# Kernel tuning notes

Measured on AMD Instinct MI355X. Metric: run time of the kernel, lower is better.

## Reference

```python
import jax, jax.numpy as jnp
import numpy as np

N_NODES = 50000
N_EDGES = 800000
IN_FEATS = 128
N_HIDDEN = 128
N_CLASSES = 64


def setup_inputs() -> dict:
    key = jax.random.key(0)
    ks = jax.random.split(key, 12)
    x = jax.random.normal(ks[0], (N_NODES, IN_FEATS), dtype=jnp.float32)
    src = jax.random.randint(ks[1], (N_EDGES,), 0, N_NODES, dtype=jnp.int32)
    dst = jax.random.randint(ks[2], (N_EDGES,), 0, N_NODES, dtype=jnp.int32)
    dims = [(IN_FEATS, N_HIDDEN), (N_HIDDEN, N_HIDDEN), (N_HIDDEN, N_CLASSES)]
    inp = {"x": x, "src": src, "dst": dst}
    for i, (din, dout) in enumerate(dims):
        s = (2.0 / (din + dout)) ** 0.5  # xavier-ish init scale
        inp[f"Wself{i}"] = jax.random.normal(ks[3 + 3 * i], (din, dout), dtype=jnp.float32) * s
        inp[f"Wneigh{i}"] = jax.random.normal(ks[4 + 3 * i], (din, dout), dtype=jnp.float32) * s
        inp[f"b{i}"] = jnp.zeros((dout,), dtype=jnp.float32)
    return inp


def _sage_conv(h, src, dst, inv_deg, Wself, Wneigh, b):
    # mean aggregation over in-neighbors: gather on src, segment-sum on dst
    agg = jax.ops.segment_sum(h[src], dst, num_segments=N_NODES)  # [N, d]
    h_neigh = agg * inv_deg[:, None]
    return h @ Wself + h_neigh @ Wneigh + b


def reference(x, src, dst, Wself0, Wneigh0, b0, Wself1, Wneigh1, b1, Wself2, Wneigh2, b2):
    # in-degree (clamped to 1, matching DGL mean aggregator), shared across layers
    deg = jax.ops.segment_sum(jnp.ones((N_EDGES,), dtype=jnp.float32), dst, num_segments=N_NODES)
    inv_deg = 1.0 / jnp.maximum(deg, 1.0)
    # dropout is identity in eval mode
    h = _sage_conv(x, src, dst, inv_deg, Wself0, Wneigh0, b0)
    h = jax.nn.relu(h)
    h = _sage_conv(h, src, dst, inv_deg, Wself1, Wneigh1, b1)
    h = jax.nn.relu(h)
    h = _sage_conv(h, src, dst, inv_deg, Wself2, Wneigh2, b2)
    return h
```

## Files before the change

### kernel.cpp

```cpp
#include <hip/hip_runtime.h>

#define N_NODES 50000
#define N_EDGES 800000
#define NB_SCAN 196
#define NODES_PER_GRP 6250
#define BUCKET_CAP 131072
#define CAST_BLOCKS 6250

typedef unsigned short ushort_t;
typedef __attribute__((ext_vector_type(8))) short  short8v;
typedef __attribute__((ext_vector_type(4))) float  float4v;
typedef __attribute__((ext_vector_type(4))) unsigned short ushort4v;
typedef __attribute__((ext_vector_type(8))) unsigned short ushort8v;
typedef __attribute__((ext_vector_type(4))) int int4v;

__device__ __forceinline__ ushort_t f2bf(float f) {
    unsigned u = __float_as_uint(f);
    unsigned r = 0x7fffu + ((u >> 16) & 1u);
    return (ushort_t)((u + r) >> 16);
}
__device__ __forceinline__ float bf2f(ushort_t h) {
    return __uint_as_float((unsigned)h << 16);
}

__global__ __launch_bounds__(256) void cast_pack_k(const float* __restrict__ x,
                                                   ushort_t* __restrict__ xb,
                                                   int* __restrict__ bcur,
                                                   const float* __restrict__ W0n, const float* __restrict__ W0s,
                                                   const float* __restrict__ W1n, const float* __restrict__ W1s,
                                                   const float* __restrict__ W2n, const float* __restrict__ W2s,
                                                   ushort_t* __restrict__ P) {
    const int b = blockIdx.x, t = threadIdx.x;
    if (b < CAST_BLOCKS) {
        int i = b * 256 + t;
        if (i < N_NODES * 32) {
            float4 v = ((const float4*)x)[i];
            ushort4v h;
            h[0] = f2bf(v.x); h[1] = f2bf(v.y); h[2] = f2bf(v.z); h[3] = f2bf(v.w);
            ((ushort4v*)xb)[i] = h;
        }
        if (i < 8) bcur[i] = 0;
        return;
    }
    int tid = (b - CAST_BLOCKS) * 256 + t;
    const float* W; int dout; int base; int r;
    if      (tid < 2048)  { W = W0n; dout = 128; base = 0;     r = tid; }
    else if (tid < 4096)  { W = W0s; dout = 128; base = 16384; r = tid - 2048; }
    else if (tid < 6144)  { W = W1n; dout = 128; base = 32768; r = tid - 4096; }
    else if (tid < 8192)  { W = W1s; dout = 128; base = 49152; r = tid - 6144; }
    else if (tid < 9216)  { W = W2n; dout = 64;  base = 65536; r = tid - 8192; }
    else                  { W = W2s; dout = 64;  base = 73728; r = tid - 9216; }
    int lane = r & 63;
    int ks = (r >> 6) & 3;
    int nt = r >> 8;
    int col = nt * 16 + (lane & 15);
    int k0 = ks * 32 + ((lane >> 4) << 3);
    ushort_t* d = P + (size_t)base + (size_t)r * 8;
    ushort4v lo4, hi4;
#pragma unroll
    for (int j = 0; j < 4; ++j) lo4[j] = f2bf(W[(size_t)(k0 + j) * dout + col]);
#pragma unroll
    for (int j = 0; j < 4; ++j) hi4[j] = f2bf(W[(size_t)(k0 + 4 + j) * dout + col]);
    *(ushort4v*)d = lo4;
    *(ushort4v*)(d + 4) = hi4;
}

__global__ __launch_bounds__(256) void bucket_k(const int4v* __restrict__ dst4,
                                                const int4v* __restrict__ src4,
                                                int* __restrict__ bcur,
                                                int2* __restrict__ buckets) {
    __shared__ int lcount[8];
    __shared__ int lbase[8];
    const int t = threadIdx.x, b = blockIdx.x;
    if (t < 8) lcount[t] = 0;
    __syncthreads();

    const int idx = b * 256 + t;
    int4v d, s;
    if (idx < N_EDGES / 4) {
        d = __builtin_nontemporal_load(dst4 + idx);
        s = __builtin_nontemporal_load(src4 + idx);
    } else {
        d[0] = d[1] = d[2] = d[3] = -1;
        s[0] = s[1] = s[2] = s[3] = 0;
    }
    int g[4], li[4];
#pragma unroll
    for (int j = 0; j < 4; ++j) {
        int dv = d[j];
        g[j] = (dv >= 0) ? (dv / NODES_PER_GRP) : -1;
        li[j] = (g[j] >= 0) ? atomicAdd(&lcount[g[j]], 1) : 0;
    }
    __syncthreads();
    if (t < 8) lbase[t] = atomicAdd(bcur + t, lcount[t]);
    __syncthreads();
#pragma unroll
    for (int j = 0; j < 4; ++j) {
        if (g[j] >= 0) {
            int pos = lbase[g[j]] + li[j];
            buckets[(size_t)g[j] * BUCKET_CAP + pos] = make_int2(d[j], s[j]);
        }
    }
}

__global__ __launch_bounds__(1024) void deg_hist_k(const int* __restrict__ bcur,
                                                   const int2* __restrict__ buckets,
                                                   int* __restrict__ deg) {
    __shared__ int hist[NODES_PER_GRP];
    const int g = blockIdx.x;
    const int t = threadIdx.x;
    const int lo = g * NODES_PER_GRP;
    const int cnt = bcur[g];
    const int2* bk = buckets + (size_t)g * BUCKET_CAP;
    for (int i = t; i < NODES_PER_GRP; i += 1024) hist[i] = 0;
    __syncthreads();
    for (int i = t; i < cnt; i += 1024) {
        atomicAdd(&hist[bk[i].x - lo], 1);
    }
    __syncthreads();
    for (int i = t; i < NODES_PER_GRP; i += 1024) deg[lo + i] = hist[i];
}

__global__ __launch_bounds__(256) void block_sum_k(const int* __restrict__ deg,
                                                   int* __restrict__ bsum, int n) {
    __shared__ int s[256];
    int t = threadIdx.x, b = blockIdx.x;
    int i = b * 256 + t;
    s[t] = (i < n) ? deg[i] : 0;
    __syncthreads();
#pragma unroll
    for (int off = 128; off > 0; off >>= 1) {
        if (t < off) s[t] += s[t + off];
        __syncthreads();
    }
    if (t == 0) bsum[b] = s[0];
}

__global__ __launch_bounds__(256) void rowptr_fused_k(const int* __restrict__ deg,
                                                      const int* __restrict__ bsum,
                                                      int* __restrict__ rowptr,
                                                      int* __restrict__ cursor,
                                                      float* __restrict__ inv) {
    __shared__ int sb[256];
    __shared__ int s[256];
    const int t = threadIdx.x, b = blockIdx.x;
    int v = (t < NB_SCAN) ? bsum[t] : 0;
    sb[t] = v;
    __syncthreads();
#pragma unroll
    for (int off = 1; off < 256; off <<= 1) {
        int u = (t >= off) ? sb[t - off] : 0;
        __syncthreads();
        sb[t] += u;
        __syncthreads();
    }
    const int boffb = (b == 0) ? 0 : sb[b - 1];
    if (b == NB_SCAN - 1 && t == 0) rowptr[N_NODES] = sb[NB_SCAN - 1];

    int i = b * 256 + t;
    int d = (i < N_NODES) ? deg[i] : 0;
    s[t] = d;
    __syncthreads();
#pragma unroll
    for (int off = 1; off < 256; off <<= 1) {
        int u = (t >= off) ? s[t - off] : 0;
        __syncthreads();
        s[t] += u;
        __syncthreads();
    }
    if (i < N_NODES) {
        int r = boffb + s[t] - d;
        rowptr[i] = r;
        cursor[i] = r;
        inv[i] = 1.0f / fmaxf((float)d, 1.0f);
    }
}

__global__ __launch_bounds__(256) void scatter_bucket_k(const int* __restrict__ bcur,
                                                        const int2* __restrict__ buckets,
                                                        int* __restrict__ cursor,
                                                        int* __restrict__ csr) {
    const int grp = blockIdx.x & 7;
    const int cnt = bcur[grp];
    const int2* bk = buckets + (size_t)grp * BUCKET_CAP;
    const int stride = (gridDim.x >> 3) * 256;
    for (int i = (blockIdx.x >> 3) * 256 + threadIdx.x; i < cnt; i += stride) {
        int2 e = bk[i];
        csr[atomicAdd(cursor + e.x, 1)] = e.y;
    }
}

__global__ __launch_bounds__(256) void aggm_k(const ushort_t* __restrict__ h,
                                              const int* __restrict__ rowptr,
                                              const int* __restrict__ csr,
                                              const float* __restrict__ inv,
                                              ushort_t* __restrict__ m, int N) {
    int node = (blockIdx.x * 256 + threadIdx.x) >> 4;
    int c = threadIdx.x & 15;
    if (node >= N) return;
    int start = rowptr[node], end = rowptr[node + 1];

    const ushort8v* hp = (const ushort8v*)h;
    float a0[8] = {}, a1[8] = {}, a2[8] = {}, a3[8] = {};
    int j = start;
    for (; j + 3 < end; j += 4) {
        int u0 = csr[j], u1 = csr[j + 1], u2 = csr[j + 2], u3 = csr[j + 3];
        ushort8v w0 = hp[(size_t)u0 * 16 + c];
        ushort8v w1 = hp[(size_t)u1 * 16 + c];
        ushort8v w2 = hp[(size_t)u2 * 16 + c];
        ushort8v w3 = hp[(size_t)u3 * 16 + c];
#pragma unroll
        for (int k = 0; k < 8; ++k) {
            a0[k] += bf2f(w0[k]); a1[k] += bf2f(w1[k]);
            a2[k] += bf2f(w2[k]); a3[k] += bf2f(w3[k]);
        }
    }
    for (; j < end; ++j) {
        ushort8v w = hp[(size_t)csr[j] * 16 + c];
#pragma unroll
        for (int k = 0; k < 8; ++k) a0[k] += bf2f(w[k]);
    }
    float s = inv[node];
    ushort8v o;
#pragma unroll
    for (int k = 0; k < 8; ++k) o[k] = f2bf(((a0[k] + a1[k]) + (a2[k] + a3[k])) * s);
    __builtin_nontemporal_store(o, (ushort8v*)m + (size_t)node * 16 + c);
}

__global__ __launch_bounds__(256, 4) void fusedgemm_k(const ushort_t* __restrict__ H,
                                                      const ushort_t* __restrict__ M,
                                                      const short8v* __restrict__ Ws,
                                                      const short8v* __restrict__ Wn,
                                                      const float* __restrict__ bias,
                                                      ushort_t* __restrict__ Out, int N) {
    __shared__ ushort_t sm[2][64 * 128];
    char* sbH = (char*)sm[0];
    char* sbM = (char*)sm[1];
    const int bm = blockIdx.x * 64;
    const int t = threadIdx.x;
    const int w = t >> 6, l = t & 63;

    {
        const ushort8v* Hp = (const ushort8v*)H;
        const ushort8v* Mp = (const ushort8v*)M;
        ushort8v zeroV = {0, 0, 0, 0, 0, 0, 0, 0};
#pragma unroll
        for (int it = 0; it < 4; ++it) {
            int r = it * 16 + (t >> 4);
            int row = bm + r;
            int byte = (r * 256 + (t & 15) * 16) ^ ((r & 7) << 4);
            ushort8v vh = zeroV, vm = zeroV;
            if (row < N) {
                vh = Hp[(size_t)row * 16 + (t & 15)];
                vm = __builtin_nontemporal_load(Mp + (size_t)row * 16 + (t & 15));
            }
            *(ushort8v*)(sbH + byte) = vh;
            *(ushort8v*)(sbM + byte) = vm;
        }
    }
    __syncthreads();

    float bv[8];
#pragma unroll
    for (int nt = 0; nt < 8; ++nt) bv[nt] = bias[nt * 16 + (l & 15)];

    float4v acc[8] = {};
#pragma unroll
    for (int ks = 0; ks < 4; ++ks) {
        int r0 = w * 16 + (l & 15);
        int b0 = (r0 * 256 + ks * 64 + (l >> 4) * 16) ^ ((r0 & 7) << 4);
        short8v ah = *(const short8v*)(sbH + b0);
        short8v am = *(const short8v*)(sbM + b0);
#pragma unroll
        for (int nt = 0; nt < 8; ++nt) {
            short8v bs = Ws[(nt * 4 + ks) * 64 + l];
            short8v bn = Wn[(nt * 4 + ks) * 64 + l];
            acc[nt] = __builtin_amdgcn_mfma_f32_16x16x32_bf16(ah, bs, acc[nt], 0, 0, 0);
            acc[nt] = __builtin_amdgcn_mfma_f32_16x16x32_bf16(am, bn, acc[nt], 0, 0, 0);
        }
    }

#pragma unroll
    for (int i = 0; i < 4; ++i) {
        int row = bm + w * 16 + (l >> 4) * 4 + i;
        if (row < N) {
#pragma unroll
            for (int nt = 0; nt < 8; ++nt) {
                int col = nt * 16 + (l & 15);
                Out[(size_t)row * 128 + col] = f2bf(fmaxf(acc[nt][i] + bv[nt], 0.f));
            }
        }
    }
}

__global__ __launch_bounds__(256, 4) void dual64_k(const ushort_t* __restrict__ A,
                                                   const short8v* __restrict__ Wn,
                                                   const short8v* __restrict__ Ws,
                                                   const float* __restrict__ bias,
                                                   ushort_t* __restrict__ Z,
                                                   float* __restrict__ S, int N) {
    constexpr int NT = 4;
    __shared__ ushort_t Asm[64 * 128];
    char* sb = (char*)Asm;
    const int bm = blockIdx.x * 64;
    const int t = threadIdx.x;
    const int w = t >> 6, l = t & 63;

    {
        const ushort8v* Ap = (const ushort8v*)A;
        ushort8v zeroV = {0, 0, 0, 0, 0, 0, 0, 0};
#pragma unroll
        for (int it = 0; it < 4; ++it) {
            int r = it * 16 + (t >> 4);
            int row = bm + r;
            ushort8v v = zeroV;
            if (row < N) v = Ap[(size_t)row * 16 + (t & 15)];
            int byte = (r * 256 + (t & 15) * 16) ^ ((r & 7) << 4);
            *(ushort8v*)(sb + byte) = v;
        }
    }
    __syncthreads();

    float bv[NT];
#pragma unroll
    for (int nt = 0; nt < NT; ++nt) bv[nt] = bias[nt * 16 + (l & 15)];

    float4v accS[NT] = {}, accN[NT] = {};
#pragma unroll
    for (int ks = 0; ks < 4; ++ks) {
        int r0 = w * 16 + (l & 15);
        int b0 = (r0 * 256 + ks * 64 + (l >> 4) * 16) ^ ((r0 & 7) << 4);
        short8v a = *(const short8v*)(sb + b0);
#pragma unroll
        for (int nt = 0; nt < NT; ++nt) {
            short8v bs = Ws[(nt * 4 + ks) * 64 + l];
            short8v bn = Wn[(nt * 4 + ks) * 64 + l];
            accS[nt] = __builtin_amdgcn_mfma_f32_16x16x32_bf16(a, bs, accS[nt], 0, 0, 0);
            accN[nt] = __builtin_amdgcn_mfma_f32_16x16x32_bf16(a, bn, accN[nt], 0, 0, 0);
        }
    }

#pragma unroll
    for (int i = 0; i < 4; ++i) {
        int row = bm + w * 16 + (l >> 4) * 4 + i;
        if (row < N) {
#pragma unroll
            for (int nt = 0; nt < NT; ++nt) {
                int col = nt * 16 + (l & 15);
                S[(size_t)row * 64 + col] = accS[nt][i] + bv[nt];
                Z[(size_t)row * 64 + col] = f2bf(accN[nt][i]);
            }
        }
    }
}

__global__ __launch_bounds__(256) void agg64_k(const ushort_t* __restrict__ z,
                                               const int* __restrict__ rowptr,
                                               const int* __restrict__ csr,
                                               const float* __restrict__ inv,
                                               float* __restrict__ out, int N) {
    int node = (blockIdx.x * 256 + threadIdx.x) >> 3;
    int c = threadIdx.x & 7;
    if (node >= N) return;
    int start = rowptr[node], end = rowptr[node + 1];

    const ushort8v* zp = (const ushort8v*)z;
    float a0[8] = {}, a1[8] = {}, a2[8] = {}, a3[8] = {};
    int j = start;
    for (; j + 3 < end; j += 4) {
        int u0 = csr[j], u1 = csr[j + 1], u2 = csr[j + 2], u3 = csr[j + 3];
        ushort8v w0 = zp[(size_t)u0 * 8 + c];
        ushort8v w1 = zp[(size_t)u1 * 8 + c];
        ushort8v w2 = zp[(size_t)u2 * 8 + c];
        ushort8v w3 = zp[(size_t)u3 * 8 + c];
#pragma unroll
        for (int k = 0; k < 8; ++k) {
            a0[k] += bf2f(w0[k]); a1[k] += bf2f(w1[k]);
            a2[k] += bf2f(w2[k]); a3[k] += bf2f(w3[k]);
        }
    }
    for (; j < end; ++j) {
        ushort8v w = zp[(size_t)csr[j] * 8 + c];
#pragma unroll
        for (int k = 0; k < 8; ++k) a0[k] += bf2f(w[k]);
    }
    float s = inv[node];
    float* op = out + (size_t)node * 64 + c * 8;
    float4 o0 = *(float4*)op;
    float4 o1 = *(float4*)(op + 4);
    o0.x += ((a0[0] + a1[0]) + (a2[0] + a3[0])) * s;
    o0.y += ((a0[1] + a1[1]) + (a2[1] + a3[1])) * s;
    o0.z += ((a0[2] + a1[2]) + (a2[2] + a3[2])) * s;
    o0.w += ((a0[3] + a1[3]) + (a2[3] + a3[3])) * s;
    o1.x += ((a0[4] + a1[4]) + (a2[4] + a3[4])) * s;
    o1.y += ((a0[5] + a1[5]) + (a2[5] + a3[5])) * s;
    o1.z += ((a0[6] + a1[6]) + (a2[6] + a3[6])) * s;
    o1.w += ((a0[7] + a1[7]) + (a2[7] + a3[7])) * s;
    *(float4*)op = o0;
    *(float4*)(op + 4) = o1;
}


extern "C" void kernel_launch(void* const* d_in, const int* in_sizes, int n_in,
                              void* d_out, int out_size, void* d_ws, size_t ws_size,
                              hipStream_t stream) {
    const float* x       = (const float*)d_in[0];
    const int*   src     = (const int*)d_in[1];
    const int*   dst     = (const int*)d_in[2];
    const float* Wself0  = (const float*)d_in[3];
    const float* Wneigh0 = (const float*)d_in[4];
    const float* b0      = (const float*)d_in[5];
    const float* Wself1  = (const float*)d_in[6];
    const float* Wneigh1 = (const float*)d_in[7];
    const float* b1      = (const float*)d_in[8];
    const float* Wself2  = (const float*)d_in[9];
    const float* Wneigh2 = (const float*)d_in[10];
    const float* b2      = (const float*)d_in[11];
    float* out = (float*)d_out;

    char* ws = (char*)d_ws;
    size_t off = 0;
    auto alloc = [&](size_t bytes) -> void* {
        void* p = ws + off;
        off += (bytes + 255) & ~(size_t)255;
        return p;
    };
    int*      deg     = (int*)alloc((size_t)N_NODES * 4);
    float*    inv     = (float*)alloc((size_t)N_NODES * 4);
    int*      rowptr  = (int*)alloc((size_t)(N_NODES + 1) * 4);
    int*      cursor  = (int*)alloc((size_t)N_NODES * 4);
    int*      csr     = (int*)alloc((size_t)N_EDGES * 4);
    int*      bsum    = (int*)alloc((size_t)NB_SCAN * 4);
    int*      bcur    = (int*)alloc((size_t)8 * 4);
    int2*     buckets = (int2*)alloc((size_t)8 * BUCKET_CAP * 8);
    ushort_t* packW   = (ushort_t*)alloc((size_t)81920 * 2);
    ushort_t* xb      = (ushort_t*)alloc((size_t)N_NODES * 128 * 2);
    ushort_t* mbuf    = (ushort_t*)alloc((size_t)N_NODES * 128 * 2);
    ushort_t* h1      = (ushort_t*)alloc((size_t)N_NODES * 128 * 2);
    ushort_t* h2      = (ushort_t*)alloc((size_t)N_NODES * 128 * 2);
    ushort_t* z64     = (ushort_t*)alloc((size_t)N_NODES * 64 * 2);

    dim3 b256(256);
    const int gemmBlocks   = (N_NODES + 63) / 64;
    const int aggmBlocks   = (N_NODES * 16 + 255) / 256;
    const int agg64Blocks  = (N_NODES * 8 + 255) / 256;
    const int bucketBlocks = (N_EDGES / 4 + 255) / 256;

    cast_pack_k<<<CAST_BLOCKS + 40, b256, 0, stream>>>(x, xb, bcur,
                                                       Wneigh0, Wself0, Wneigh1, Wself1,
                                                       Wneigh2, Wself2, packW);
    bucket_k<<<bucketBlocks, b256, 0, stream>>>((const int4v*)dst, (const int4v*)src,
                                                bcur, buckets);
    deg_hist_k<<<8, dim3(1024), 0, stream>>>(bcur, buckets, deg);
    block_sum_k<<<NB_SCAN, b256, 0, stream>>>(deg, bsum, N_NODES);
    rowptr_fused_k<<<NB_SCAN, b256, 0, stream>>>(deg, bsum, rowptr, cursor, inv);
    scatter_bucket_k<<<512, b256, 0, stream>>>(bcur, buckets, cursor, csr);

    const short8v* pN0 = (const short8v*)(packW);
    const short8v* pS0 = (const short8v*)(packW + 16384);
    const short8v* pN1 = (const short8v*)(packW + 32768);
    const short8v* pS1 = (const short8v*)(packW + 49152);
    const short8v* pN2 = (const short8v*)(packW + 65536);
    const short8v* pS2 = (const short8v*)(packW + 73728);

    aggm_k<<<aggmBlocks, b256, 0, stream>>>(xb, rowptr, csr, inv, mbuf, N_NODES);
    fusedgemm_k<<<gemmBlocks, b256, 0, stream>>>(xb, mbuf, pS0, pN0, b0, h1, N_NODES);

    aggm_k<<<aggmBlocks, b256, 0, stream>>>(h1, rowptr, csr, inv, mbuf, N_NODES);
    fusedgemm_k<<<gemmBlocks, b256, 0, stream>>>(h1, mbuf, pS1, pN1, b1, h2, N_NODES);

    dual64_k<<<gemmBlocks, b256, 0, stream>>>(h2, pN2, pS2, b2, z64, out, N_NODES);
    agg64_k<<<agg64Blocks, b256, 0, stream>>>(z64, rowptr, csr, inv, out, N_NODES);
}
```

Measured before the change: 218.3 us.

## Fuse neighbor mean-aggregation into GEMM kernel and fold block sums into histogram

Replaces the separate aggregation kernel plus GEMM with one kernel that gathers and averages neighbor rows directly into shared memory before the MFMA loop, eliminating the intermediate aggregated buffer write and read and one launch per layer. Also computes the per-256-node degree block sums inside the histogram kernel by regrouping nodes into 6400-node buckets, removing the block_sum kernel. The fused kernel runs the irregular gather with fewer blocks and serializes gather with compute, which may reduce latency hiding.

```diff
diff --git a/kernel.cpp b/kernel.cpp
--- a/kernel.cpp
+++ b/kernel.cpp
@@ -3,7 +3,8 @@
 #define N_NODES 50000
 #define N_EDGES 800000
 #define NB_SCAN 196
-#define NODES_PER_GRP 6250
+#define NODES_PER_GRP 6400
+#define CHUNKS_PER_GRP 25
 #define BUCKET_CAP 131072
 #define CAST_BLOCKS 6250
 
@@ -105,7 +106,8 @@
 
 __global__ __launch_bounds__(1024) void deg_hist_k(const int* __restrict__ bcur,
                                                    const int2* __restrict__ buckets,
-                                                   int* __restrict__ deg) {
+                                                   int* __restrict__ deg,
+                                                   int* __restrict__ bsum) {
     __shared__ int hist[NODES_PER_GRP];
     const int g = blockIdx.x;
     const int t = threadIdx.x;
@@ -118,22 +120,17 @@
         atomicAdd(&hist[bk[i].x - lo], 1);
     }
     __syncthreads();
-    for (int i = t; i < NODES_PER_GRP; i += 1024) deg[lo + i] = hist[i];
-}
-
-__global__ __launch_bounds__(256) void block_sum_k(const int* __restrict__ deg,
-                                                   int* __restrict__ bsum, int n) {
-    __shared__ int s[256];
-    int t = threadIdx.x, b = blockIdx.x;
-    int i = b * 256 + t;
-    s[t] = (i < n) ? deg[i] : 0;
-    __syncthreads();
-#pragma unroll
-    for (int off = 128; off > 0; off >>= 1) {
-        if (t < off) s[t] += s[t + off];
-        __syncthreads();
-    }
-    if (t == 0) bsum[b] = s[0];
+    const int nNodes = (N_NODES - lo < NODES_PER_GRP) ? (N_NODES - lo) : NODES_PER_GRP;
+    for (int i = t; i < nNodes; i += 1024) deg[lo + i] = hist[i];
+    const int wave = t >> 6, lane = t & 63;
+    const int nch = (nNodes + 255) >> 8;
+    for (int c = wave; c < nch; c += 16) {
+        int base = c * 256 + lane;
+        int s = hist[base] + hist[base + 64] + hist[base + 128] + hist[base + 192];
+#pragma unroll
+        for (int off = 32; off > 0; off >>= 1) s += __shfl_xor(s, off);
+        if (lane == 0) bsum[g * CHUNKS_PER_GRP + c] = s;
+    }
 }
 
 __global__ __launch_bounds__(256) void rowptr_fused_k(const int* __restrict__ deg,
@@ -190,73 +187,66 @@
     }
 }
 
-__global__ __launch_bounds__(256) void aggm_k(const ushort_t* __restrict__ h,
-                                              const int* __restrict__ rowptr,
-                                              const int* __restrict__ csr,
-                                              const float* __restrict__ inv,
-                                              ushort_t* __restrict__ m, int N) {
-    int node = (blockIdx.x * 256 + threadIdx.x) >> 4;
-    int c = threadIdx.x & 15;
-    if (node >= N) return;
-    int start = rowptr[node], end = rowptr[node + 1];
-
-    const ushort8v* hp = (const ushort8v*)h;
-    float a0[8] = {}, a1[8] = {}, a2[8] = {}, a3[8] = {};
-    int j = start;
-    for (; j + 3 < end; j += 4) {
-        int u0 = csr[j], u1 = csr[j + 1], u2 = csr[j + 2], u3 = csr[j + 3];
-        ushort8v w0 = hp[(size_t)u0 * 16 + c];
-        ushort8v w1 = hp[(size_t)u1 * 16 + c];
-        ushort8v w2 = hp[(size_t)u2 * 16 + c];
-        ushort8v w3 = hp[(size_t)u3 * 16 + c];
-#pragma unroll
-        for (int k = 0; k < 8; ++k) {
-            a0[k] += bf2f(w0[k]); a1[k] += bf2f(w1[k]);
-            a2[k] += bf2f(w2[k]); a3[k] += bf2f(w3[k]);
-        }
-    }
-    for (; j < end; ++j) {
-        ushort8v w = hp[(size_t)csr[j] * 16 + c];
-#pragma unroll
-        for (int k = 0; k < 8; ++k) a0[k] += bf2f(w[k]);
-    }
-    float s = inv[node];
-    ushort8v o;
-#pragma unroll
-    for (int k = 0; k < 8; ++k) o[k] = f2bf(((a0[k] + a1[k]) + (a2[k] + a3[k])) * s);
-    __builtin_nontemporal_store(o, (ushort8v*)m + (size_t)node * 16 + c);
-}
-
-__global__ __launch_bounds__(256, 4) void fusedgemm_k(const ushort_t* __restrict__ H,
-                                                      const ushort_t* __restrict__ M,
-                                                      const short8v* __restrict__ Ws,
-                                                      const short8v* __restrict__ Wn,
-                                                      const float* __restrict__ bias,
-                                                      ushort_t* __restrict__ Out, int N) {
+__global__ __launch_bounds__(256, 4) void gathergemm_k(const ushort_t* __restrict__ H,
+                                                       const int* __restrict__ rowptr,
+                                                       const int* __restrict__ csr,
+                                                       const float* __restrict__ inv,
+                                                       const short8v* __restrict__ Ws,
+                                                       const short8v* __restrict__ Wn,
+                                                       const float* __restrict__ bias,
+                                                       ushort_t* __restrict__ Out, int N) {
     __shared__ ushort_t sm[2][64 * 128];
     char* sbH = (char*)sm[0];
     char* sbM = (char*)sm[1];
     const int bm = blockIdx.x * 64;
     const int t = threadIdx.x;
     const int w = t >> 6, l = t & 63;
-
-    {
-        const ushort8v* Hp = (const ushort8v*)H;
-        const ushort8v* Mp = (const ushort8v*)M;
-        ushort8v zeroV = {0, 0, 0, 0, 0, 0, 0, 0};
-#pragma unroll
-        for (int it = 0; it < 4; ++it) {
-            int r = it * 16 + (t >> 4);
-            int row = bm + r;
-            int byte = (r * 256 + (t & 15) * 16) ^ ((r & 7) << 4);
-            ushort8v vh = zeroV, vm = zeroV;
-            if (row < N) {
-                vh = Hp[(size_t)row * 16 + (t & 15)];
-                vm = __builtin_nontemporal_load(Mp + (size_t)row * 16 + (t & 15));
+    const ushort8v* Hp = (const ushort8v*)H;
+    ushort8v zeroV = {0, 0, 0, 0, 0, 0, 0, 0};
+
+#pragma unroll
+    for (int it = 0; it < 4; ++it) {
+        int r = it * 16 + (t >> 4);
+        int row = bm + r;
+        int byte = (r * 256 + (t & 15) * 16) ^ ((r & 7) << 4);
+        ushort8v vh = zeroV;
+        if (row < N) vh = Hp[(size_t)row * 16 + (t & 15)];
+        *(ushort8v*)(sbH + byte) = vh;
+    }
+
+    const int c = t & 15;
+#pragma unroll
+    for (int pass = 0; pass < 4; ++pass) {
+        int r = pass * 16 + (t >> 4);
+        int row = bm + r;
+        int byte = (r * 256 + c * 16) ^ ((r & 7) << 4);
+        ushort8v o = zeroV;
+        if (row < N) {
+            int start = rowptr[row], end = rowptr[row + 1];
+            float a0[8] = {}, a1[8] = {}, a2[8] = {}, a3[8] = {};
+            int j = start;
+            for (; j + 3 < end; j += 4) {
+                int u0 = csr[j], u1 = csr[j + 1], u2 = csr[j + 2], u3 = csr[j + 3];
+                ushort8v w0 = Hp[(size_t)u0 * 16 + c];
+                ushort8v w1 = Hp[(size_t)u1 * 16 + c];
+                ushort8v w2 = Hp[(size_t)u2 * 16 + c];
+                ushort8v w3 = Hp[(size_t)u3 * 16 + c];
+#pragma unroll
+                for (int k = 0; k < 8; ++k) {
+                    a0[k] += bf2f(w0[k]); a1[k] += bf2f(w1[k]);
+                    a2[k] += bf2f(w2[k]); a3[k] += bf2f(w3[k]);
+                }
             }
-            *(ushort8v*)(sbH + byte) = vh;
-            *(ushort8v*)(sbM + byte) = vm;
-        }
+            for (; j < end; ++j) {
+                ushort8v wv = Hp[(size_t)csr[j] * 16 + c];
+#pragma unroll
+                for (int k = 0; k < 8; ++k) a0[k] += bf2f(wv[k]);
+            }
+            float sc = inv[row];
+#pragma unroll
+            for (int k = 0; k < 8; ++k) o[k] = f2bf(((a0[k] + a1[k]) + (a2[k] + a3[k])) * sc);
+        }
+        *(ushort8v*)(sbM + byte) = o;
     }
     __syncthreads();
 
@@ -435,14 +425,12 @@
     int2*     buckets = (int2*)alloc((size_t)8 * BUCKET_CAP * 8);
     ushort_t* packW   = (ushort_t*)alloc((size_t)81920 * 2);
     ushort_t* xb      = (ushort_t*)alloc((size_t)N_NODES * 128 * 2);
-    ushort_t* mbuf    = (ushort_t*)alloc((size_t)N_NODES * 128 * 2);
     ushort_t* h1      = (ushort_t*)alloc((size_t)N_NODES * 128 * 2);
     ushort_t* h2      = (ushort_t*)alloc((size_t)N_NODES * 128 * 2);
     ushort_t* z64     = (ushort_t*)alloc((size_t)N_NODES * 64 * 2);
 
     dim3 b256(256);
     const int gemmBlocks   = (N_NODES + 63) / 64;
-    const int aggmBlocks   = (N_NODES * 16 + 255) / 256;
     const int agg64Blocks  = (N_NODES * 8 + 255) / 256;
     const int bucketBlocks = (N_EDGES / 4 + 255) / 256;
 
@@ -451,8 +439,7 @@
                                                        Wneigh2, Wself2, packW);
     bucket_k<<<bucketBlocks, b256, 0, stream>>>((const int4v*)dst, (const int4v*)src,
                                                 bcur, buckets);
-    deg_hist_k<<<8, dim3(1024), 0, stream>>>(bcur, buckets, deg);
-    block_sum_k<<<NB_SCAN, b256, 0, stream>>>(deg, bsum, N_NODES);
+    deg_hist_k<<<8, dim3(1024), 0, stream>>>(bcur, buckets, deg, bsum);
     rowptr_fused_k<<<NB_SCAN, b256, 0, stream>>>(deg, bsum, rowptr, cursor, inv);
     scatter_bucket_k<<<512, b256, 0, stream>>>(bcur, buckets, cursor, csr);
 
@@ -463,11 +450,9 @@
     const short8v* pN2 = (const short8v*)(packW + 65536);
     const short8v* pS2 = (const short8v*)(packW + 73728);
 
-    aggm_k<<<aggmBlocks, b256, 0, stream>>>(xb, rowptr, csr, inv, mbuf, N_NODES);
-    fusedgemm_k<<<gemmBlocks, b256, 0, stream>>>(xb, mbuf, pS0, pN0, b0, h1, N_NODES);
-
-    aggm_k<<<aggmBlocks, b256, 0, stream>>>(h1, rowptr, csr, inv, mbuf, N_NODES);
-    fusedgemm_k<<<gemmBlocks, b256, 0, stream>>>(h1, mbuf, pS1, pN1, b1, h2, N_NODES);
+    gathergemm_k<<<gemmBlocks, b256, 0, stream>>>(xb, rowptr, csr, inv, pS0, pN0, b0, h1, N_NODES);
+
+    gathergemm_k<<<gemmBlocks, b256, 0, stream>>>(h1, rowptr, csr, inv, pS1, pN1, b1, h2, N_NODES);
 
     dual64_k<<<gemmBlocks, b256, 0, stream>>>(h2, pN2, pS2, b2, z64, out, N_NODES);
     agg64_k<<<agg64Blocks, b256, 0, stream>>>(z64, rowptr, csr, inv, out, N_NODES);
```

Measured after the change: 211.7 us. 3.1% less time.
